# Optimization experiments

Hardware: AMD Instinct MI355X
Metric: run time of the kernel (lower is better)

## Reference

```python
import jax, jax.numpy as jnp
import numpy as np

TEMPERATURE = 0.1  # matches init kwarg


def _l2_normalize(x):
    # tf.math.l2_normalize along axis=1
    return x / jnp.sqrt(jnp.sum(x * x, axis=1, keepdims=True))


def _nearest_neighbour(p, queue):
    # brute-force top-1 retrieval: [B,D] @ [D,Q] -> argmax -> gather
    sims = p @ queue.T                      # [B, Q]
    nn = queue[jnp.argmax(sims, axis=1)]    # [B, D]
    return p + jax.lax.stop_gradient(nn - p)


def setup_inputs() -> dict:
    key = jax.random.key(0)
    k1, k2, k3 = jax.random.split(key, 3)
    B, Q, D = 4096, 32768, 128
    return {
        "projections_1": jax.random.normal(k1, (B, D), dtype=jnp.float32),
        "projections_2": jax.random.normal(k2, (B, D), dtype=jnp.float32),
        "feature_queue": _l2_normalize(jax.random.normal(k3, (Q, D), dtype=jnp.float32)),
    }


def reference(projections_1, projections_2, feature_queue):
    p1 = _l2_normalize(projections_1)
    p2 = _l2_normalize(projections_2)
    n1 = _nearest_neighbour(p1, feature_queue)
    n2 = _nearest_neighbour(p2, feature_queue)
    t = TEMPERATURE
    s_1_2_1 = (n1 @ p2.T) / t   # [B, B]
    s_1_2_2 = (p2 @ n1.T) / t
    s_2_1_1 = (n2 @ p1.T) / t
    s_2_1_2 = (p1 @ n2.T) / t
    logits = jnp.concatenate([s_1_2_1, s_1_2_2, s_2_1_1, s_2_1_2], axis=0)  # [4B, B]
    B = p1.shape[0]
    labels = jnp.tile(jnp.arange(B), 4)  # [4B]
    log_probs = jax.nn.log_softmax(logits, axis=1)
    # sparse categorical crossentropy per row (from_logits=True)
    loss = -jnp.take_along_axis(log_probs, labels[:, None], axis=1)[:, 0]
    return loss
```

## Files before the change

### kernel.cpp

```cpp
#include <hip/hip_runtime.h>
#include <math.h>


#define B_N 4096
#define D_N 128
#define NP 8192
#define NTILE 512
#define INV_T 10.0f
#define C1F (10.0f * 1.4426950408889634f)
#define C2F (16.0f * 1.4426950408889634f)
#define W_WIN 8e-3f

typedef _Float16 half8 __attribute__((ext_vector_type(8)));
typedef __fp16 fp16x2 __attribute__((ext_vector_type(2)));
typedef float f32x4 __attribute__((ext_vector_type(4)));
union H8 { half8 v; fp16x2 h2[4]; };

#define OFF_PH 0u
#define OFF_QH 2097152u
#define OFF_NH 2097152u
#define OFF_TV 6291456u
#define OFF_DG 6291456u
#define OFF_SP 6324224u
#define OFF_RM1 14680064u
#define OFF_RM 14942208u
#define OFF_KEY 14974976u

__device__ __forceinline__ void gload16(const void* g, void* l) {
  __builtin_amdgcn_global_load_lds((const __attribute__((address_space(1))) void*)g,
                                   (__attribute__((address_space(3))) void*)l, 16, 0, 0);
}

__global__ __launch_bounds__(256) void k_normalize(const float* __restrict__ in1,
                                                   const float* __restrict__ in2,
                                                   _Float16* __restrict__ Ph) {
  int t = threadIdx.x, w = t >> 6, l = t & 63;
  int g = blockIdx.x * 4 + w;
  int view = g >> 12, row = g & (B_N - 1);
  const float* src = (view ? in2 : in1) + (size_t)row * D_N;
  float2 v = *(const float2*)(src + 2 * l);
  float ss = fmaf(v.x, v.x, v.y * v.y);
#pragma unroll
  for (int m = 1; m < 64; m <<= 1) ss += __shfl_xor(ss, m);
  float rn = 1.0f / sqrtf(ss);
  *(fp16x2*)(Ph + (size_t)g * D_N + 2 * l) = __builtin_amdgcn_cvt_pkrtz(v.x * rn, v.y * rn);
}

__global__ __launch_bounds__(256) void k_qcvt(const float* __restrict__ src,
                                              _Float16* __restrict__ dst) {
  int i = blockIdx.x * 256 + threadIdx.x;
  const float* s = src + (size_t)i * 8;
  float4 x = *(const float4*)s;
  float4 y = *(const float4*)(s + 4);
  H8 h;
  h.h2[0] = __builtin_amdgcn_cvt_pkrtz(x.x, x.y);
  h.h2[1] = __builtin_amdgcn_cvt_pkrtz(x.z, x.w);
  h.h2[2] = __builtin_amdgcn_cvt_pkrtz(y.x, y.y);
  h.h2[3] = __builtin_amdgcn_cvt_pkrtz(y.z, y.w);
  *(half8*)(dst + (size_t)i * 8) = h.v;
}

__global__ __launch_bounds__(256, 2) void k_nn(const _Float16* __restrict__ Qh,
                                               const _Float16* __restrict__ Ph,
                                               _Float16* __restrict__ tv, int h) {
  __shared__ _Float16 sm[2][16384];
  int bid = blockIdx.x;
  int c2 = bid & 7, pb = bid >> 3;
  int t = threadIdx.x, l = t & 63, w = t >> 6;
  int wq = w >> 1, wp = w & 1, l15 = l & 15, l4 = l >> 4;
  half8 Pf4[4][4];
  const _Float16* pbase = Ph + (size_t)(pb * 128 + wp * 64 + l15) * D_N + l4 * 8;
#pragma unroll
  for (int tj = 0; tj < 4; ++tj)
#pragma unroll
    for (int ks = 0; ks < 4; ++ks)
      Pf4[tj][ks] = *(const half8*)(pbase + (size_t)tj * 16 * D_N + ks * 32);
  int tidb = h * 256 + c2 * 32;
  int pcol = pb * 128 + wp * 64 + l15;
  {
    int qrow0 = c2 * 2048;
#pragma unroll
    for (int j = 0; j < 8; ++j) {
      int r = ((w * 8 + j) << 2) + l4;
      const _Float16* src = Qh + ((size_t)(qrow0 + r) << 7) + ((l15 ^ (r & 7)) << 3);
      gload16(src, (char*)(&sm[0][0]) + ((w * 8 + j) << 10));
    }
  }
#pragma unroll 1
  for (int qt = 0; qt < 16; ++qt) {
    int cur = qt & 1;
    __syncthreads();
    if (qt + 1 < 16) {
      int qrow0 = c2 * 2048 + (qt + 1) * 128;
#pragma unroll
      for (int j = 0; j < 8; ++j) {
        int r = ((w * 8 + j) << 2) + l4;
        const _Float16* src = Qh + ((size_t)(qrow0 + r) << 7) + ((l15 ^ (r & 7)) << 3);
        gload16(src, (char*)(&sm[cur ^ 1][0]) + ((w * 8 + j) << 10));
      }
    }
    const char* bb = (const char*)(&sm[cur][0]);
    f32x4 acc[4][4];
#pragma unroll
    for (int i = 0; i < 4; ++i)
#pragma unroll
      for (int j = 0; j < 4; ++j) acc[i][j] = (f32x4){0.f, 0.f, 0.f, 0.f};
#pragma unroll
    for (int ks = 0; ks < 4; ++ks) {
      half8 Qf[4];
#pragma unroll
      for (int ti = 0; ti < 4; ++ti) {
        int qloc = wq * 64 + ti * 16 + l15;
        int byteo = qloc * 256 + ((((ks << 2) + l4) ^ (qloc & 7)) << 4);
        Qf[ti] = *(const half8*)(bb + byteo);
      }
#pragma unroll
      for (int ti = 0; ti < 4; ++ti)
#pragma unroll
        for (int tj = 0; tj < 4; ++tj)
          acc[ti][tj] =
              __builtin_amdgcn_mfma_f32_16x16x32_f16(Qf[ti], Pf4[tj][ks], acc[ti][tj], 0, 0, 0);
    }
    int tid = tidb + qt * 2 + wq;
#pragma unroll
    for (int tj = 0; tj < 4; ++tj) {
      float m = acc[0][tj][0];
#pragma unroll
      for (int ti = 0; ti < 4; ++ti)
#pragma unroll
        for (int r = 0; r < 4; ++r) m = fmaxf(m, acc[ti][tj][r]);
      m = fmaxf(m, __shfl_xor(m, 16));
      m = fmaxf(m, __shfl_xor(m, 32));
      if (l4 == 0) tv[(size_t)tid * NP + pcol + tj * 16] = (_Float16)m;
    }
  }
}

__global__ __launch_bounds__(256) void k_rowmax1(const _Float16* __restrict__ tv,
                                                 float* __restrict__ rm1) {
  int p = blockIdx.x * 256 + threadIdx.x;
  int g = blockIdx.y;
  float m = -3e38f;
  for (int tid = g * 64; tid < g * 64 + 64; ++tid) m = fmaxf(m, (float)tv[(size_t)tid * NP + p]);
  rm1[(size_t)g * NP + p] = m;
}

__global__ __launch_bounds__(256) void k_rowmax2(const float* __restrict__ rm1,
                                                 float* __restrict__ rowmax,
                                                 unsigned long long* __restrict__ keys) {
  int p = blockIdx.x * 256 + threadIdx.x;
  float m = rm1[p];
#pragma unroll
  for (int g = 1; g < 8; ++g) m = fmaxf(m, rm1[(size_t)g * NP + p]);
  rowmax[p] = m;
  keys[p] = 0ull;
}

__global__ __launch_bounds__(256) void k_rescore(const float* __restrict__ queue,
                                                 const float* __restrict__ in1,
                                                 const float* __restrict__ in2,
                                                 const _Float16* __restrict__ tv,
                                                 const float* __restrict__ rowmax,
                                                 unsigned long long* __restrict__ keys) {
  __shared__ float Qs[64][132];
  __shared__ unsigned short cand[NP];
  __shared__ int cnt;
  int tile = blockIdx.x;
  int t = threadIdx.x;
  if (t == 0) cnt = 0;
  __syncthreads();
  int qbase = tile << 6;
#pragma unroll
  for (int j = 0; j < 8; ++j) {
    int i = j * 256 + t;
    int r = i >> 5, c = i & 31;
    *(float4*)(&Qs[r][c << 2]) = *(const float4*)(queue + ((size_t)(qbase + r) << 7) + (c << 2));
  }
  const _Float16* tvrow = tv + (size_t)tile * NP;
#pragma unroll
  for (int j = 0; j < 32; ++j) {
    int p = j * 256 + t;
    float v = (float)tvrow[p];
    if (v >= rowmax[p] - W_WIN) {
      int k = atomicAdd(&cnt, 1);
      cand[k] = (unsigned short)p;
    }
  }
  __syncthreads();
  int n = cnt;
  int w = t >> 6, l = t & 63;
  for (int ci = w; ci < n; ci += 4) {
    int p = cand[ci];
    const float* prow = (p < B_N) ? (in1 + ((size_t)p << 7)) : (in2 + ((size_t)(p - B_N) << 7));
    float d = 0.f;
#pragma unroll
    for (int k = 0; k < 32; ++k) {
      float4 a = *(const float4*)(prow + (k << 2));
      float4 b = *(const float4*)(&Qs[l][k << 2]);
      d = fmaf(a.x, b.x, d);
      d = fmaf(a.y, b.y, d);
      d = fmaf(a.z, b.z, d);
      d = fmaf(a.w, b.w, d);
    }
    int idx = qbase + l;
#pragma unroll
    for (int m = 1; m < 64; m <<= 1) {
      float ov = __shfl_xor(d, m);
      int oi = __shfl_xor(idx, m);
      if (ov > d || (ov == d && oi < idx)) {
        d = ov;
        idx = oi;
      }
    }
    if (l == 0) {
      unsigned u = __float_as_uint(d);
      u = ((int)u < 0) ? ~u : (u | 0x80000000u);
      unsigned long long key = ((unsigned long long)u << 32) | (unsigned)(~idx);
      atomicMax(keys + p, key);
    }
  }
}

__global__ __launch_bounds__(256) void k_gather(const float* __restrict__ queue,
                                                const float* __restrict__ in1,
                                                const float* __restrict__ in2,
                                                const unsigned long long* __restrict__ keys,
                                                _Float16* __restrict__ Nh,
                                                float* __restrict__ diag) {
  int t = threadIdx.x, w = t >> 6, l = t & 63;
  int g = blockIdx.x * 4 + w;
  int view = g >> 12, row = g & (B_N - 1);
  unsigned long long key = keys[g];
  int qidx = (int)(~(unsigned)(key & 0xffffffffull));
  const float* q = queue + (size_t)qidx * D_N;
  float2 qv = *(const float2*)(q + 2 * l);
  *(fp16x2*)(Nh + (size_t)g * D_N + 2 * l) = __builtin_amdgcn_cvt_pkrtz(qv.x, qv.y);
  const float* oth = (view ? in1 : in2) + (size_t)row * D_N;
  float2 ov = *(const float2*)(oth + 2 * l);
  float ss = fmaf(ov.x, ov.x, ov.y * ov.y);
  float d = fmaf(qv.x, ov.x, qv.y * ov.y);
#pragma unroll
  for (int m = 1; m < 64; m <<= 1) {
    ss += __shfl_xor(ss, m);
    d += __shfl_xor(d, m);
  }
  if (l == 0) diag[g] = d / sqrtf(ss);
}

__global__ __launch_bounds__(256, 2) void k_loss(const _Float16* __restrict__ Ph,
                                                 const _Float16* __restrict__ Nh,
                                                 float* __restrict__ Spart) {
  __shared__ _Float16 sm[2][16384];
  __shared__ float sred[2][2][64];
  int rb = blockIdx.x;
  int chunk = blockIdx.y;
  int pair = rb >> 5, rowblk = rb & 31;
  const size_t BDh = (size_t)B_N * D_N;
  const _Float16* A = (pair == 0) ? Nh : (pair == 1) ? (Ph + BDh) : (pair == 2) ? (Nh + BDh) : Ph;
  const _Float16* Bm = (pair == 0) ? (Ph + BDh) : (pair == 1) ? Nh : (pair == 2) ? Ph : (Nh + BDh);
  int t = threadIdx.x, l = t & 63, w = t >> 6;
  int wr = w >> 1, wc = w & 1, l15 = l & 15, l4 = l >> 4;
  half8 Af[4][4];
  const _Float16* ab = A + (size_t)(rowblk * 128 + wr * 64 + l15) * D_N + l4 * 8;
#pragma unroll
  for (int ti = 0; ti < 4; ++ti)
#pragma unroll
    for (int ks = 0; ks < 4; ++ks)
      Af[ti][ks] = *(const half8*)(ab + (size_t)ti * 16 * D_N + ks * 32);
  float S[16];
#pragma unroll
  for (int i = 0; i < 16; ++i) S[i] = 0.f;
  {
    int crow0 = chunk * 1024;
#pragma unroll
    for (int j = 0; j < 8; ++j) {
      int r = ((w * 8 + j) << 2) + l4;
      const _Float16* src = Bm + ((size_t)(crow0 + r) << 7) + ((l15 ^ (r & 7)) << 3);
      gload16(src, (char*)(&sm[0][0]) + ((w * 8 + j) << 10));
    }
  }
#pragma unroll 1
  for (int ct = 0; ct < 8; ++ct) {
    int cur = ct & 1;
    __syncthreads();
    if (ct + 1 < 8) {
      int crow0 = chunk * 1024 + (ct + 1) * 128;
#pragma unroll
      for (int j = 0; j < 8; ++j) {
        int r = ((w * 8 + j) << 2) + l4;
        const _Float16* src = Bm + ((size_t)(crow0 + r) << 7) + ((l15 ^ (r & 7)) << 3);
        gload16(src, (char*)(&sm[cur ^ 1][0]) + ((w * 8 + j) << 10));
      }
    }
    const char* bbp = (const char*)(&sm[cur][0]);
    f32x4 acc[4][4];
#pragma unroll
    for (int i = 0; i < 4; ++i)
#pragma unroll
      for (int j = 0; j < 4; ++j) acc[i][j] = (f32x4){0.f, 0.f, 0.f, 0.f};
#pragma unroll
    for (int ks = 0; ks < 4; ++ks) {
      half8 Bf[4];
#pragma unroll
      for (int tj = 0; tj < 4; ++tj) {
        int bloc = wc * 64 + tj * 16 + l15;
        int byteo = bloc * 256 + ((((ks << 2) + l4) ^ (bloc & 7)) << 4);
        Bf[tj] = *(const half8*)(bbp + byteo);
      }
#pragma unroll
      for (int ti = 0; ti < 4; ++ti)
#pragma unroll
        for (int tj = 0; tj < 4; ++tj)
          acc[ti][tj] =
              __builtin_amdgcn_mfma_f32_16x16x32_f16(Af[ti][ks], Bf[tj], acc[ti][tj], 0, 0, 0);
    }
#pragma unroll
    for (int ti = 0; ti < 4; ++ti)
#pragma unroll
      for (int r = 0; r < 4; ++r) {
        float e = 0.f;
#pragma unroll
        for (int tj = 0; tj < 4; ++tj) e += exp2f(fmaf(acc[ti][tj][r], C1F, -C2F));
        S[ti * 4 + r] += e;
      }
  }
#pragma unroll
  for (int i = 0; i < 16; ++i) {
#pragma unroll
    for (int m = 1; m < 16; m <<= 1) S[i] += __shfl_xor(S[i], m);
  }
  __syncthreads();
  if (l15 == 0) {
#pragma unroll
    for (int ti = 0; ti < 4; ++ti)
#pragma unroll
      for (int r = 0; r < 4; ++r) sred[wr][wc][ti * 16 + l4 * 4 + r] = S[ti * 4 + r];
  }
  __syncthreads();
  if (t < 128) {
    int wrr = t >> 6, rl = t & 63;
    float s = sred[wrr][0][rl] + sred[wrr][1][rl];
    int row = pair * B_N + rowblk * 128 + wrr * 64 + rl;
    Spart[(size_t)row * 4 + chunk] = s;
  }
}

__global__ __launch_bounds__(256) void k_merge(const float* __restrict__ Spart,
                                               const float* __restrict__ diag,
                                               float* __restrict__ out) {
  int row = blockIdx.x * 256 + threadIdx.x;
  const float* sp = Spart + (size_t)row * 4;
  float s = sp[0] + sp[1] + sp[2] + sp[3];
  int pair = row >> 12, r = row & (B_N - 1);
  float dg = diag[(pair >> 1) * B_N + r];
  out[row] = logf(s) + 16.0f - INV_T * dg;
}

extern "C" void kernel_launch(void* const* d_in, const int* in_sizes, int n_in,
                              void* d_out, int out_size, void* d_ws, size_t ws_size,
                              hipStream_t stream) {
  const float* in1 = (const float*)d_in[0];
  const float* in2 = (const float*)d_in[1];
  const float* queue = (const float*)d_in[2];
  float* out = (float*)d_out;
  char* ws = (char*)d_ws;
  _Float16* Ph = (_Float16*)(ws + OFF_PH);
  _Float16* Qhh = (_Float16*)(ws + OFF_QH);
  _Float16* Nh = (_Float16*)(ws + OFF_NH);
  _Float16* TV = (_Float16*)(ws + OFF_TV);
  float* DG = (float*)(ws + OFF_DG);
  float* SP = (float*)(ws + OFF_SP);
  float* RM1 = (float*)(ws + OFF_RM1);
  float* RM = (float*)(ws + OFF_RM);
  unsigned long long* KEY = (unsigned long long*)(ws + OFF_KEY);

  hipLaunchKernelGGL(k_normalize, dim3(2048), dim3(256), 0, stream, in1, in2, Ph);
  for (int h = 0; h < 2; ++h) {
    hipLaunchKernelGGL(k_qcvt, dim3(1024), dim3(256), 0, stream, queue + (size_t)h * 16384 * D_N,
                       Qhh);
    hipLaunchKernelGGL(k_nn, dim3(512), dim3(256), 0, stream, Qhh, Ph, TV, h);
  }
  hipLaunchKernelGGL(k_rowmax1, dim3(32, 8), dim3(256), 0, stream, TV, RM1);
  hipLaunchKernelGGL(k_rowmax2, dim3(32), dim3(256), 0, stream, RM1, RM, KEY);
  hipLaunchKernelGGL(k_rescore, dim3(512), dim3(256), 0, stream, queue, in1, in2, TV, RM, KEY);
  hipLaunchKernelGGL(k_gather, dim3(2048), dim3(256), 0, stream, queue, in1, in2, KEY, Nh, DG);
  hipLaunchKernelGGL(k_loss, dim3(128, 4), dim3(256), 0, stream, Ph, Nh, SP);
  hipLaunchKernelGGL(k_merge, dim3(64), dim3(256), 0, stream, SP, DG, out);
}
```

Measured before the change: 180.1 us.

## Retile NN and loss GEMMs to 128-column register tiles, single-pass queue

The NN-search and loss kernels now hold all 128 columns of the P/A operand in registers per wave (8 fragments) and stream 64-row tiles of the other operand through LDS, so each wave reads one LDS fragment per k-step instead of four. Per-tile maxima are reduced across waves via a small shared buffer and written one stage late. The queue is converted to fp16 in a single pass with a larger workspace, which removes the two-half loop and one launch pair. Rescore is split across two blocks per tile to expose more parallelism. The larger register-resident operand raises register pressure, and the extra per-stage syncs may hurt occupancy.

```diff
diff --git a/kernel.cpp b/kernel.cpp
--- a/kernel.cpp
+++ b/kernel.cpp
@@ -18,13 +18,13 @@
 
 #define OFF_PH 0u
 #define OFF_QH 2097152u
-#define OFF_NH 2097152u
-#define OFF_TV 6291456u
-#define OFF_DG 6291456u
-#define OFF_SP 6324224u
-#define OFF_RM1 14680064u
-#define OFF_RM 14942208u
-#define OFF_KEY 14974976u
+#define OFF_NH 10485760u
+#define OFF_TV 12582912u
+#define OFF_RM1 20971520u
+#define OFF_RM 21233664u
+#define OFF_KEY 21266432u
+#define OFF_DG 21331968u
+#define OFF_SP 21364736u
 
 __device__ __forceinline__ void gload16(const void* g, void* l) {
   __builtin_amdgcn_global_load_lds((const __attribute__((address_space(1))) void*)g,
@@ -60,79 +60,72 @@
   *(half8*)(dst + (size_t)i * 8) = h.v;
 }
 
+#define STAGE64(MAT, RB, BUF)                                                  \
+  {                                                                            \
+    _Pragma("unroll") for (int j = 0; j < 4; ++j) {                            \
+      int ch = w * 4 + j;                                                      \
+      int r = (ch << 2) + l4;                                                  \
+      gload16(MAT + (((RB) + r) << 7) + ((l15 ^ (r & 7)) << 3),                \
+              (char*)(&sm[BUF][0]) + (ch << 10));                              \
+    }                                                                          \
+  }
+
 __global__ __launch_bounds__(256, 2) void k_nn(const _Float16* __restrict__ Qh,
                                                const _Float16* __restrict__ Ph,
-                                               _Float16* __restrict__ tv, int h) {
-  __shared__ _Float16 sm[2][16384];
+                                               _Float16* __restrict__ tv) {
+  __shared__ _Float16 sm[2][8192];
+  __shared__ float smax[2][4][128];
   int bid = blockIdx.x;
-  int c2 = bid & 7, pb = bid >> 3;
+  int qc = (bid & 7) | ((bid >> 9) << 3);
+  int pb = (bid >> 3) & 63;
   int t = threadIdx.x, l = t & 63, w = t >> 6;
-  int wq = w >> 1, wp = w & 1, l15 = l & 15, l4 = l >> 4;
-  half8 Pf4[4][4];
-  const _Float16* pbase = Ph + (size_t)(pb * 128 + wp * 64 + l15) * D_N + l4 * 8;
-#pragma unroll
-  for (int tj = 0; tj < 4; ++tj)
+  int l15 = l & 15, l4 = l >> 4;
+  half8 Pf4[8][4];
+  const _Float16* pbase = Ph + (size_t)(pb * 128 + l15) * D_N + l4 * 8;
+#pragma unroll
+  for (int fr = 0; fr < 8; ++fr)
 #pragma unroll
     for (int ks = 0; ks < 4; ++ks)
-      Pf4[tj][ks] = *(const half8*)(pbase + (size_t)tj * 16 * D_N + ks * 32);
-  int tidb = h * 256 + c2 * 32;
-  int pcol = pb * 128 + wp * 64 + l15;
-  {
-    int qrow0 = c2 * 2048;
-#pragma unroll
-    for (int j = 0; j < 8; ++j) {
-      int r = ((w * 8 + j) << 2) + l4;
-      const _Float16* src = Qh + ((size_t)(qrow0 + r) << 7) + ((l15 ^ (r & 7)) << 3);
-      gload16(src, (char*)(&sm[0][0]) + ((w * 8 + j) << 10));
-    }
-  }
+      Pf4[fr][ks] = *(const half8*)(pbase + (size_t)(fr * 16) * D_N + ks * 32);
+  const size_t qrow0 = (size_t)qc * 2048;
+  STAGE64(Qh, qrow0, 0)
 #pragma unroll 1
-  for (int qt = 0; qt < 16; ++qt) {
-    int cur = qt & 1;
+  for (int s = 0; s < 32; ++s) {
+    int cur = s & 1;
     __syncthreads();
-    if (qt + 1 < 16) {
-      int qrow0 = c2 * 2048 + (qt + 1) * 128;
-#pragma unroll
-      for (int j = 0; j < 8; ++j) {
-        int r = ((w * 8 + j) << 2) + l4;
-        const _Float16* src = Qh + ((size_t)(qrow0 + r) << 7) + ((l15 ^ (r & 7)) << 3);
-        gload16(src, (char*)(&sm[cur ^ 1][0]) + ((w * 8 + j) << 10));
-      }
+    if (s < 31) STAGE64(Qh, qrow0 + (s + 1) * 64, cur ^ 1)
+    if (s > 0 && t < 128) {
+      int sp = s - 1, par = sp & 1;
+      float v = fmaxf(fmaxf(smax[par][0][t], smax[par][1][t]),
+                      fmaxf(smax[par][2][t], smax[par][3][t]));
+      tv[(size_t)(qc * 32 + sp) * NP + pb * 128 + t] = (_Float16)v;
     }
     const char* bb = (const char*)(&sm[cur][0]);
-    f32x4 acc[4][4];
-#pragma unroll
-    for (int i = 0; i < 4; ++i)
-#pragma unroll
-      for (int j = 0; j < 4; ++j) acc[i][j] = (f32x4){0.f, 0.f, 0.f, 0.f};
+    f32x4 acc[8];
+#pragma unroll
+    for (int fr = 0; fr < 8; ++fr) acc[fr] = (f32x4){0.f, 0.f, 0.f, 0.f};
 #pragma unroll
     for (int ks = 0; ks < 4; ++ks) {
-      half8 Qf[4];
-#pragma unroll
-      for (int ti = 0; ti < 4; ++ti) {
-        int qloc = wq * 64 + ti * 16 + l15;
-        int byteo = qloc * 256 + ((((ks << 2) + l4) ^ (qloc & 7)) << 4);
-        Qf[ti] = *(const half8*)(bb + byteo);
-      }
-#pragma unroll
-      for (int ti = 0; ti < 4; ++ti)
-#pragma unroll
-        for (int tj = 0; tj < 4; ++tj)
-          acc[ti][tj] =
-              __builtin_amdgcn_mfma_f32_16x16x32_f16(Qf[ti], Pf4[tj][ks], acc[ti][tj], 0, 0, 0);
-    }
-    int tid = tidb + qt * 2 + wq;
-#pragma unroll
-    for (int tj = 0; tj < 4; ++tj) {
-      float m = acc[0][tj][0];
-#pragma unroll
-      for (int ti = 0; ti < 4; ++ti)
-#pragma unroll
-        for (int r = 0; r < 4; ++r) m = fmaxf(m, acc[ti][tj][r]);
+      int qloc = w * 16 + l15;
+      int byteo = qloc * 256 + ((((ks << 2) + l4) ^ (qloc & 7)) << 4);
+      half8 Qf = *(const half8*)(bb + byteo);
+#pragma unroll
+      for (int fr = 0; fr < 8; ++fr)
+        acc[fr] = __builtin_amdgcn_mfma_f32_16x16x32_f16(Qf, Pf4[fr][ks], acc[fr], 0, 0, 0);
+    }
+#pragma unroll
+    for (int fr = 0; fr < 8; ++fr) {
+      float m = fmaxf(fmaxf(acc[fr][0], acc[fr][1]), fmaxf(acc[fr][2], acc[fr][3]));
       m = fmaxf(m, __shfl_xor(m, 16));
       m = fmaxf(m, __shfl_xor(m, 32));
-      if (l4 == 0) tv[(size_t)tid * NP + pcol + tj * 16] = (_Float16)m;
-    }
+      if (l < 16) smax[cur][w][fr * 16 + l] = m;
+    }
+  }
+  __syncthreads();
+  if (t < 128) {
+    float v = fmaxf(fmaxf(smax[1][0][t], smax[1][1][t]),
+                    fmaxf(smax[1][2][t], smax[1][3][t]));
+    tv[(size_t)(qc * 32 + 31) * NP + pb * 128 + t] = (_Float16)v;
   }
 }
 
@@ -162,16 +155,15 @@
                                                  const _Float16* __restrict__ tv,
                                                  const float* __restrict__ rowmax,
                                                  unsigned long long* __restrict__ keys) {
-  __shared__ float Qs[64][132];
+  __shared__ float Qs[32][132];
   __shared__ unsigned short cand[NP];
   __shared__ int cnt;
-  int tile = blockIdx.x;
-  int t = threadIdx.x;
+  int tile = blockIdx.x, qh = blockIdx.y, t = threadIdx.x;
   if (t == 0) cnt = 0;
   __syncthreads();
-  int qbase = tile << 6;
-#pragma unroll
-  for (int j = 0; j < 8; ++j) {
+  int qbase = tile * 64 + qh * 32;
+#pragma unroll
+  for (int j = 0; j < 4; ++j) {
     int i = j * 256 + t;
     int r = i >> 5, c = i & 31;
     *(float4*)(&Qs[r][c << 2]) = *(const float4*)(queue + ((size_t)(qbase + r) << 7) + (c << 2));
@@ -188,23 +180,23 @@
   }
   __syncthreads();
   int n = cnt;
-  int w = t >> 6, l = t & 63;
-  for (int ci = w; ci < n; ci += 4) {
+  int w = t >> 6, l = t & 63, hl = l >> 5, ll = l & 31;
+  for (int ci = w * 2 + hl; ci < n; ci += 8) {
     int p = cand[ci];
     const float* prow = (p < B_N) ? (in1 + ((size_t)p << 7)) : (in2 + ((size_t)(p - B_N) << 7));
     float d = 0.f;
 #pragma unroll
     for (int k = 0; k < 32; ++k) {
       float4 a = *(const float4*)(prow + (k << 2));
-      float4 b = *(const float4*)(&Qs[l][k << 2]);
+      float4 b = *(const float4*)(&Qs[ll][k << 2]);
       d = fmaf(a.x, b.x, d);
       d = fmaf(a.y, b.y, d);
       d = fmaf(a.z, b.z, d);
       d = fmaf(a.w, b.w, d);
     }
-    int idx = qbase + l;
-#pragma unroll
-    for (int m = 1; m < 64; m <<= 1) {
+    int idx = qbase + ll;
+#pragma unroll
+    for (int m = 1; m < 32; m <<= 1) {
       float ov = __shfl_xor(d, m);
       int oi = __shfl_xor(idx, m);
       if (ov > d || (ov == d && oi < idx)) {
@@ -212,7 +204,7 @@
         idx = oi;
       }
     }
-    if (l == 0) {
+    if (ll == 0) {
       unsigned u = __float_as_uint(d);
       u = ((int)u < 0) ? ~u : (u | 0x80000000u);
       unsigned long long key = ((unsigned long long)u << 32) | (unsigned)(~idx);
@@ -250,8 +242,8 @@
 __global__ __launch_bounds__(256, 2) void k_loss(const _Float16* __restrict__ Ph,
                                                  const _Float16* __restrict__ Nh,
                                                  float* __restrict__ Spart) {
-  __shared__ _Float16 sm[2][16384];
-  __shared__ float sred[2][2][64];
+  __shared__ _Float16 sm[2][8192];
+  __shared__ float smat[4][128];
   int rb = blockIdx.x;
   int chunk = blockIdx.y;
   int pair = rb >> 5, rowblk = rb & 31;
@@ -259,88 +251,61 @@
   const _Float16* A = (pair == 0) ? Nh : (pair == 1) ? (Ph + BDh) : (pair == 2) ? (Nh + BDh) : Ph;
   const _Float16* Bm = (pair == 0) ? (Ph + BDh) : (pair == 1) ? Nh : (pair == 2) ? Ph : (Nh + BDh);
   int t = threadIdx.x, l = t & 63, w = t >> 6;
-  int wr = w >> 1, wc = w & 1, l15 = l & 15, l4 = l >> 4;
-  half8 Af[4][4];
-  const _Float16* ab = A + (size_t)(rowblk * 128 + wr * 64 + l15) * D_N + l4 * 8;
-#pragma unroll
-  for (int ti = 0; ti < 4; ++ti)
+  int l15 = l & 15, l4 = l >> 4;
+  half8 Af[8][4];
+  const _Float16* ab = A + (size_t)(rowblk * 128 + l15) * D_N + l4 * 8;
+#pragma unroll
+  for (int fr = 0; fr < 8; ++fr)
 #pragma unroll
     for (int ks = 0; ks < 4; ++ks)
-      Af[ti][ks] = *(const half8*)(ab + (size_t)ti * 16 * D_N + ks * 32);
-  float S[16];
-#pragma unroll
-  for (int i = 0; i < 16; ++i) S[i] = 0.f;
-  {
-    int crow0 = chunk * 1024;
-#pragma unroll
-    for (int j = 0; j < 8; ++j) {
-      int r = ((w * 8 + j) << 2) + l4;
-      const _Float16* src = Bm + ((size_t)(crow0 + r) << 7) + ((l15 ^ (r & 7)) << 3);
-      gload16(src, (char*)(&sm[0][0]) + ((w * 8 + j) << 10));
-    }
-  }
+      Af[fr][ks] = *(const half8*)(ab + (size_t)(fr * 16) * D_N + ks * 32);
+  float S[8][4];
+#pragma unroll
+  for (int fr = 0; fr < 8; ++fr)
+#pragma unroll
+    for (int r = 0; r < 4; ++r) S[fr][r] = 0.f;
+  const size_t crow0 = (size_t)chunk * 1024;
+  STAGE64(Bm, crow0, 0)
 #pragma unroll 1
-  for (int ct = 0; ct < 8; ++ct) {
+  for (int ct = 0; ct < 16; ++ct) {
     int cur = ct & 1;
     __syncthreads();
-    if (ct + 1 < 8) {
-      int crow0 = chunk * 1024 + (ct + 1) * 128;
-#pragma unroll
-      for (int j = 0; j < 8; ++j) {
-        int r = ((w * 8 + j) << 2) + l4;
-        const _Float16* src = Bm + ((size_t)(crow0 + r) << 7) + ((l15 ^ (r & 7)) << 3);
-        gload16(src, (char*)(&sm[cur ^ 1][0]) + ((w * 8 + j) << 10));
-      }
-    }
-    const char* bbp = (const char*)(&sm[cur][0]);
-    f32x4 acc[4][4];
-#pragma unroll
-    for (int i = 0; i < 4; ++i)
-#pragma unroll
-      for (int j = 0; j < 4; ++j) acc[i][j] = (f32x4){0.f, 0.f, 0.f, 0.f};
+    if (ct < 15) STAGE64(Bm, crow0 + (ct + 1) * 64, cur ^ 1)
+    const char* bb = (const char*)(&sm[cur][0]);
+    f32x4 acc[8];
+#pragma unroll
+    for (int fr = 0; fr < 8; ++fr) acc[fr] = (f32x4){0.f, 0.f, 0.f, 0.f};
 #pragma unroll
     for (int ks = 0; ks < 4; ++ks) {
-      half8 Bf[4];
-#pragma unroll
-      for (int tj = 0; tj < 4; ++tj) {
-        int bloc = wc * 64 + tj * 16 + l15;
-        int byteo = bloc * 256 + ((((ks << 2) + l4) ^ (bloc & 7)) << 4);
-        Bf[tj] = *(const half8*)(bbp + byteo);
-      }
-#pragma unroll
-      for (int ti = 0; ti < 4; ++ti)
-#pragma unroll
-        for (int tj = 0; tj < 4; ++tj)
-          acc[ti][tj] =
-              __builtin_amdgcn_mfma_f32_16x16x32_f16(Af[ti][ks], Bf[tj], acc[ti][tj], 0, 0, 0);
-    }
-#pragma unroll
-    for (int ti = 0; ti < 4; ++ti)
-#pragma unroll
-      for (int r = 0; r < 4; ++r) {
-        float e = 0.f;
-#pragma unroll
-        for (int tj = 0; tj < 4; ++tj) e += exp2f(fmaf(acc[ti][tj][r], C1F, -C2F));
-        S[ti * 4 + r] += e;
-      }
-  }
-#pragma unroll
-  for (int i = 0; i < 16; ++i) {
-#pragma unroll
-    for (int m = 1; m < 16; m <<= 1) S[i] += __shfl_xor(S[i], m);
-  }
-  __syncthreads();
+      int bloc = w * 16 + l15;
+      int byteo = bloc * 256 + ((((ks << 2) + l4) ^ (bloc & 7)) << 4);
+      half8 Bf = *(const half8*)(bb + byteo);
+#pragma unroll
+      for (int fr = 0; fr < 8; ++fr)
+        acc[fr] = __builtin_amdgcn_mfma_f32_16x16x32_f16(Af[fr][ks], Bf, acc[fr], 0, 0, 0);
+    }
+#pragma unroll
+    for (int fr = 0; fr < 8; ++fr)
+#pragma unroll
+      for (int r = 0; r < 4; ++r) S[fr][r] += exp2f(fmaf(acc[fr][r], C1F, -C2F));
+  }
+#pragma unroll
+  for (int fr = 0; fr < 8; ++fr)
+#pragma unroll
+    for (int r = 0; r < 4; ++r) {
+#pragma unroll
+      for (int m = 1; m < 16; m <<= 1) S[fr][r] += __shfl_xor(S[fr][r], m);
+    }
   if (l15 == 0) {
 #pragma unroll
-    for (int ti = 0; ti < 4; ++ti)
-#pragma unroll
-      for (int r = 0; r < 4; ++r) sred[wr][wc][ti * 16 + l4 * 4 + r] = S[ti * 4 + r];
+    for (int fr = 0; fr < 8; ++fr)
+#pragma unroll
+      for (int r = 0; r < 4; ++r) smat[w][fr * 16 + l4 * 4 + r] = S[fr][r];
   }
   __syncthreads();
   if (t < 128) {
-    int wrr = t >> 6, rl = t & 63;
-    float s = sred[wrr][0][rl] + sred[wrr][1][rl];
-    int row = pair * B_N + rowblk * 128 + wrr * 64 + rl;
+    float s = smat[0][t] + smat[1][t] + smat[2][t] + smat[3][t];
+    int row = pair * B_N + rowblk * 128 + t;
     Spart[(size_t)row * 4 + chunk] = s;
   }
 }
@@ -368,21 +333,18 @@
   _Float16* Qhh = (_Float16*)(ws + OFF_QH);
   _Float16* Nh = (_Float16*)(ws + OFF_NH);
   _Float16* TV = (_Float16*)(ws + OFF_TV);
-  float* DG = (float*)(ws + OFF_DG);
-  float* SP = (float*)(ws + OFF_SP);
   float* RM1 = (float*)(ws + OFF_RM1);
   float* RM = (float*)(ws + OFF_RM);
   unsigned long long* KEY = (unsigned long long*)(ws + OFF_KEY);
+  float* DG = (float*)(ws + OFF_DG);
+  float* SP = (float*)(ws + OFF_SP);
 
   hipLaunchKernelGGL(k_normalize, dim3(2048), dim3(256), 0, stream, in1, in2, Ph);
-  for (int h = 0; h < 2; ++h) {
-    hipLaunchKernelGGL(k_qcvt, dim3(1024), dim3(256), 0, stream, queue + (size_t)h * 16384 * D_N,
-                       Qhh);
-    hipLaunchKernelGGL(k_nn, dim3(512), dim3(256), 0, stream, Qhh, Ph, TV, h);
-  }
+  hipLaunchKernelGGL(k_qcvt, dim3(2048), dim3(256), 0, stream, queue, Qhh);
+  hipLaunchKernelGGL(k_nn, dim3(1024), dim3(256), 0, stream, Qhh, Ph, TV);
   hipLaunchKernelGGL(k_rowmax1, dim3(32, 8), dim3(256), 0, stream, TV, RM1);
   hipLaunchKernelGGL(k_rowmax2, dim3(32), dim3(256), 0, stream, RM1, RM, KEY);
-  hipLaunchKernelGGL(k_rescore, dim3(512), dim3(256), 0, stream, queue, in1, in2, TV, RM, KEY);
+  hipLaunchKernelGGL(k_rescore, dim3(512, 2), dim3(256), 0, stream, queue, in1, in2, TV, RM, KEY);
   hipLaunchKernelGGL(k_gather, dim3(2048), dim3(256), 0, stream, queue, in1, in2, KEY, Nh, DG);
   hipLaunchKernelGGL(k_loss, dim3(128, 4), dim3(256), 0, stream, Ph, Nh, SP);
   hipLaunchKernelGGL(k_merge, dim3(64), dim3(256), 0, stream, SP, DG, out);
```

Result: slower. 222.3 us (+23.4%).

## Convert full queue once, run single k_nn launch, split rescore across two half-warps

Applied to the files above, without the earlier changes.

The queue is now converted to fp16 in one pass into a larger workspace region, and k_nn runs as a single 1024-block launch instead of two sequential convert+search halves. This removes two kernel launches and the serialisation between halves. k_rescore gets a second grid dimension so each block handles 32 queue rows, with each half-wave scoring a different candidate. That doubles the block count and halves per-candidate shuffle depth, but candidate filtering over the TV row is now done twice. A staging macro refactors the shared-memory loads.

```diff
diff --git a/kernel.cpp b/kernel.cpp
--- a/kernel.cpp
+++ b/kernel.cpp
@@ -18,13 +18,13 @@
 
 #define OFF_PH 0u
 #define OFF_QH 2097152u
-#define OFF_NH 2097152u
-#define OFF_TV 6291456u
-#define OFF_DG 6291456u
-#define OFF_SP 6324224u
-#define OFF_RM1 14680064u
-#define OFF_RM 14942208u
-#define OFF_KEY 14974976u
+#define OFF_NH 10485760u
+#define OFF_TV 12582912u
+#define OFF_RM1 20971520u
+#define OFF_RM 21233664u
+#define OFF_KEY 21266432u
+#define OFF_DG 21331968u
+#define OFF_SP 21364736u
 
 __device__ __forceinline__ void gload16(const void* g, void* l) {
   __builtin_amdgcn_global_load_lds((const __attribute__((address_space(1))) void*)g,
@@ -60,12 +60,23 @@
   *(half8*)(dst + (size_t)i * 8) = h.v;
 }
 
+#define STAGE128(MAT, RB, BUF)                                                 \
+  {                                                                            \
+    _Pragma("unroll") for (int j = 0; j < 8; ++j) {                            \
+      int ch = w * 8 + j;                                                      \
+      int r = (ch << 2) + l4;                                                  \
+      gload16(MAT + (((RB) + r) << 7) + ((l15 ^ (r & 7)) << 3),                \
+              (char*)(&sm[BUF][0]) + (ch << 10));                              \
+    }                                                                          \
+  }
+
 __global__ __launch_bounds__(256, 2) void k_nn(const _Float16* __restrict__ Qh,
                                                const _Float16* __restrict__ Ph,
-                                               _Float16* __restrict__ tv, int h) {
+                                               _Float16* __restrict__ tv) {
   __shared__ _Float16 sm[2][16384];
   int bid = blockIdx.x;
-  int c2 = bid & 7, pb = bid >> 3;
+  int qc = (bid & 7) | ((bid >> 9) << 3);
+  int pb = (bid >> 3) & 63;
   int t = threadIdx.x, l = t & 63, w = t >> 6;
   int wq = w >> 1, wp = w & 1, l15 = l & 15, l4 = l >> 4;
   half8 Pf4[4][4];
@@ -75,30 +86,15 @@
 #pragma unroll
     for (int ks = 0; ks < 4; ++ks)
       Pf4[tj][ks] = *(const half8*)(pbase + (size_t)tj * 16 * D_N + ks * 32);
-  int tidb = h * 256 + c2 * 32;
+  const size_t qrow0 = (size_t)qc * 2048;
+  int tidb = qc * 32;
   int pcol = pb * 128 + wp * 64 + l15;
-  {
-    int qrow0 = c2 * 2048;
-#pragma unroll
-    for (int j = 0; j < 8; ++j) {
-      int r = ((w * 8 + j) << 2) + l4;
-      const _Float16* src = Qh + ((size_t)(qrow0 + r) << 7) + ((l15 ^ (r & 7)) << 3);
-      gload16(src, (char*)(&sm[0][0]) + ((w * 8 + j) << 10));
-    }
-  }
+  STAGE128(Qh, qrow0, 0)
 #pragma unroll 1
   for (int qt = 0; qt < 16; ++qt) {
     int cur = qt & 1;
     __syncthreads();
-    if (qt + 1 < 16) {
-      int qrow0 = c2 * 2048 + (qt + 1) * 128;
-#pragma unroll
-      for (int j = 0; j < 8; ++j) {
-        int r = ((w * 8 + j) << 2) + l4;
-        const _Float16* src = Qh + ((size_t)(qrow0 + r) << 7) + ((l15 ^ (r & 7)) << 3);
-        gload16(src, (char*)(&sm[cur ^ 1][0]) + ((w * 8 + j) << 10));
-      }
-    }
+    if (qt < 15) STAGE128(Qh, qrow0 + (qt + 1) * 128, cur ^ 1)
     const char* bb = (const char*)(&sm[cur][0]);
     f32x4 acc[4][4];
 #pragma unroll
@@ -162,16 +158,15 @@
                                                  const _Float16* __restrict__ tv,
                                                  const float* __restrict__ rowmax,
                                                  unsigned long long* __restrict__ keys) {
-  __shared__ float Qs[64][132];
+  __shared__ float Qs[32][132];
   __shared__ unsigned short cand[NP];
   __shared__ int cnt;
-  int tile = blockIdx.x;
-  int t = threadIdx.x;
+  int tile = blockIdx.x, qh = blockIdx.y, t = threadIdx.x;
   if (t == 0) cnt = 0;
   __syncthreads();
-  int qbase = tile << 6;
-#pragma unroll
-  for (int j = 0; j < 8; ++j) {
+  int qbase = tile * 64 + qh * 32;
+#pragma unroll
+  for (int j = 0; j < 4; ++j) {
     int i = j * 256 + t;
     int r = i >> 5, c = i & 31;
     *(float4*)(&Qs[r][c << 2]) = *(const float4*)(queue + ((size_t)(qbase + r) << 7) + (c << 2));
@@ -188,23 +183,23 @@
   }
   __syncthreads();
   int n = cnt;
-  int w = t >> 6, l = t & 63;
-  for (int ci = w; ci < n; ci += 4) {
+  int w = t >> 6, l = t & 63, hl = l >> 5, ll = l & 31;
+  for (int ci = w * 2 + hl; ci < n; ci += 8) {
     int p = cand[ci];
     const float* prow = (p < B_N) ? (in1 + ((size_t)p << 7)) : (in2 + ((size_t)(p - B_N) << 7));
     float d = 0.f;
 #pragma unroll
     for (int k = 0; k < 32; ++k) {
       float4 a = *(const float4*)(prow + (k << 2));
-      float4 b = *(const float4*)(&Qs[l][k << 2]);
+      float4 b = *(const float4*)(&Qs[ll][k << 2]);
       d = fmaf(a.x, b.x, d);
       d = fmaf(a.y, b.y, d);
       d = fmaf(a.z, b.z, d);
       d = fmaf(a.w, b.w, d);
     }
-    int idx = qbase + l;
-#pragma unroll
-    for (int m = 1; m < 64; m <<= 1) {
+    int idx = qbase + ll;
+#pragma unroll
+    for (int m = 1; m < 32; m <<= 1) {
       float ov = __shfl_xor(d, m);
       int oi = __shfl_xor(idx, m);
       if (ov > d || (ov == d && oi < idx)) {
@@ -212,7 +207,7 @@
         idx = oi;
       }
     }
-    if (l == 0) {
+    if (ll == 0) {
       unsigned u = __float_as_uint(d);
       u = ((int)u < 0) ? ~u : (u | 0x80000000u);
       unsigned long long key = ((unsigned long long)u << 32) | (unsigned)(~idx);
@@ -270,28 +265,13 @@
   float S[16];
 #pragma unroll
   for (int i = 0; i < 16; ++i) S[i] = 0.f;
-  {
-    int crow0 = chunk * 1024;
-#pragma unroll
-    for (int j = 0; j < 8; ++j) {
-      int r = ((w * 8 + j) << 2) + l4;
-      const _Float16* src = Bm + ((size_t)(crow0 + r) << 7) + ((l15 ^ (r & 7)) << 3);
-      gload16(src, (char*)(&sm[0][0]) + ((w * 8 + j) << 10));
-    }
-  }
+  const size_t crow0 = (size_t)chunk * 1024;
+  STAGE128(Bm, crow0, 0)
 #pragma unroll 1
   for (int ct = 0; ct < 8; ++ct) {
     int cur = ct & 1;
     __syncthreads();
-    if (ct + 1 < 8) {
-      int crow0 = chunk * 1024 + (ct + 1) * 128;
-#pragma unroll
-      for (int j = 0; j < 8; ++j) {
-        int r = ((w * 8 + j) << 2) + l4;
-        const _Float16* src = Bm + ((size_t)(crow0 + r) << 7) + ((l15 ^ (r & 7)) << 3);
-        gload16(src, (char*)(&sm[cur ^ 1][0]) + ((w * 8 + j) << 10));
-      }
-    }
+    if (ct < 7) STAGE128(Bm, crow0 + (ct + 1) * 128, cur ^ 1)
     const char* bbp = (const char*)(&sm[cur][0]);
     f32x4 acc[4][4];
 #pragma unroll
@@ -368,21 +348,18 @@
   _Float16* Qhh = (_Float16*)(ws + OFF_QH);
   _Float16* Nh = (_Float16*)(ws + OFF_NH);
   _Float16* TV = (_Float16*)(ws + OFF_TV);
-  float* DG = (float*)(ws + OFF_DG);
-  float* SP = (float*)(ws + OFF_SP);
   float* RM1 = (float*)(ws + OFF_RM1);
   float* RM = (float*)(ws + OFF_RM);
   unsigned long long* KEY = (unsigned long long*)(ws + OFF_KEY);
+  float* DG = (float*)(ws + OFF_DG);
+  float* SP = (float*)(ws + OFF_SP);
 
   hipLaunchKernelGGL(k_normalize, dim3(2048), dim3(256), 0, stream, in1, in2, Ph);
-  for (int h = 0; h < 2; ++h) {
-    hipLaunchKernelGGL(k_qcvt, dim3(1024), dim3(256), 0, stream, queue + (size_t)h * 16384 * D_N,
-                       Qhh);
-    hipLaunchKernelGGL(k_nn, dim3(512), dim3(256), 0, stream, Qhh, Ph, TV, h);
-  }
+  hipLaunchKernelGGL(k_qcvt, dim3(2048), dim3(256), 0, stream, queue, Qhh);
+  hipLaunchKernelGGL(k_nn, dim3(1024), dim3(256), 0, stream, Qhh, Ph, TV);
   hipLaunchKernelGGL(k_rowmax1, dim3(32, 8), dim3(256), 0, stream, TV, RM1);
   hipLaunchKernelGGL(k_rowmax2, dim3(32), dim3(256), 0, stream, RM1, RM, KEY);
-  hipLaunchKernelGGL(k_rescore, dim3(512), dim3(256), 0, stream, queue, in1, in2, TV, RM, KEY);
+  hipLaunchKernelGGL(k_rescore, dim3(512, 2), dim3(256), 0, stream, queue, in1, in2, TV, RM, KEY);
   hipLaunchKernelGGL(k_gather, dim3(2048), dim3(256), 0, stream, queue, in1, in2, KEY, Nh, DG);
   hipLaunchKernelGGL(k_loss, dim3(128, 4), dim3(256), 0, stream, Ph, Nh, SP);
   hipLaunchKernelGGL(k_merge, dim3(64), dim3(256), 0, stream, SP, DG, out);
```

Measured after the change: 172.5 us. 4.2% less time.
